# Performance work log

Hardware: AMD Instinct MI355X
Metric: run time of the kernel (lower is better)

Reference implementation:

```python
import jax, jax.numpy as jnp
import numpy as np

B, S, C = 2, 2048, 1536
HQ, HKV = 16, 4
DQK, DV = 128, 96
MAX_POS = 2048
CLIP = 5.0
EPS = 1e-5


def layer_norm(x, g, b):
    mu = jnp.mean(x, axis=-1, keepdims=True)
    var = jnp.mean(jnp.square(x - mu), axis=-1, keepdims=True)
    return (x - mu) * jax.lax.rsqrt(var + EPS) * g + b


def rms_bn(x, g, ms):
    # eval-mode EMA RMS batch-norm: per-channel running mean-square `ms`
    return x * jax.lax.rsqrt(ms + EPS) * g


def rope(x):
    # x: [B, S, H, C] with C even
    c = x.shape[-1]
    nf = c // 2
    s = x.shape[1]
    positions = jnp.arange(s, dtype=x.dtype)
    lin = jnp.arange(nf, dtype=x.dtype)
    end = max(MAX_POS - nf + 1.0, 1.0)
    geom = jnp.exp(jnp.linspace(0.0, jnp.log(jnp.asarray(end, dtype=x.dtype)), nf))
    inv_freq = 1.0 / (lin + geom)
    theta = positions[:, None] * inv_freq          # [S, nf]
    theta = jnp.repeat(theta, 2, axis=-1)[:, None, :]  # [S, 1, C]
    x_rot = jnp.stack([-x[..., 1::2], x[..., ::2]], axis=-1).reshape(x.shape)
    return x * jnp.cos(theta) + x_rot * jnp.sin(theta)


def setup_inputs() -> dict:
    key = jax.random.key(0)
    ks = jax.random.split(key, 8)
    d = {
        'x': jax.random.normal(ks[0], (B, S, C), dtype=jnp.float32),
        'bn1_g': jnp.ones((C,), jnp.float32),
        'bn1_ms': jnp.ones((C,), jnp.float32),
        'Wq': jax.random.normal(ks[1], (C, HQ * DQK), jnp.float32) * 0.02,
        'Wk': jax.random.normal(ks[2], (C, HKV * DQK), jnp.float32) * 0.02,
        'Wv': jax.random.normal(ks[3], (C, HKV * DV), jnp.float32) * 0.02,
        'qn_g': jnp.ones((DQK,), jnp.float32), 'qn_b': jnp.zeros((DQK,), jnp.float32),
        'kn_g': jnp.ones((DQK,), jnp.float32), 'kn_b': jnp.zeros((DQK,), jnp.float32),
        'vn_g': jnp.ones((DV,), jnp.float32), 'vn_b': jnp.zeros((DV,), jnp.float32),
        'Wo': jax.random.normal(ks[4], (HQ * DV, C), jnp.float32) * 0.02,
        'bo': jnp.zeros((C,), jnp.float32),
        'bn2_g': jnp.ones((C,), jnp.float32),
        'bn2_ms': jnp.ones((C,), jnp.float32),
    }
    return d


def reference(x, bn1_g, bn1_ms, Wq, Wk, Wv, qn_g, qn_b, kn_g, kn_b, vn_g, vn_b, Wo, bo, bn2_g, bn2_ms):
    rep = HQ // HKV
    h = rms_bn(x, bn1_g, bn1_ms)                       # [B,S,C]
    q = (h @ Wq).reshape(B, S, HQ, DQK)
    k = (h @ Wk).reshape(B, S, HKV, DQK)
    v = (h @ Wv).reshape(B, S, HKV, DV)
    q = layer_norm(q, qn_g, qn_b)
    k = layer_norm(k, kn_g, kn_b)
    v = layer_norm(v, vn_g, vn_b)
    q = rope(q)
    k = rope(k)
    # torch .repeat(1,1,rep,1) tiles head axis: [h0..hkv-1] * rep
    k = jnp.tile(k, (1, 1, rep, 1))                    # [B,S,HQ,DQK]
    v = jnp.tile(v, (1, 1, rep, 1))                    # [B,S,HQ,DV]
    logits = jnp.einsum('bshc,bShc->bhsS', q, k) / (DQK ** 0.5)
    logits = jnp.tanh(logits / CLIP) * CLIP
    attn = jax.nn.softmax(logits, axis=-1)
    y = jnp.einsum('bhsS,bShc->bshc', attn, v)         # [B,S,HQ,DV]
    y = y.reshape(B, S, HQ * DV)
    y = y @ Wo + bo
    y = rms_bn(y, bn2_g, bn2_ms)
    return y
```

## Files before the change

### kernel.cpp

```cpp
#include <hip/hip_runtime.h>
#include <hip/hip_bf16.h>
#include <math.h>

typedef __hip_bfloat16 bf16;
typedef __attribute__((ext_vector_type(8))) short short8;
typedef __attribute__((ext_vector_type(4))) short short4s;
typedef __attribute__((ext_vector_type(4))) float f32x4;

constexpr int Bb=2, Ss=2048, Cc=1536, HQn=16, HKVn=4, Dqk=128, Dv=96;
constexpr int NR   = Bb*Ss;
constexpr int NQKV = HQn*Dqk + HKVn*Dqk + HKVn*Dv;
constexpr int COL_K = HQn*Dqk;
constexpr int COL_V = COL_K + HKVn*Dqk;
constexpr int NY   = HQn*Dv;
constexpr float EPSf=1e-5f, CLIPf=5.0f;
constexpr float LOG2E = 1.44269504089f;

__device__ __forceinline__ float s2f(short s) {
    unsigned u = ((unsigned)(unsigned short)s) << 16;
    return __builtin_bit_cast(float, u);
}
__device__ __forceinline__ short f2s(float v) {
    bf16 b = __float2bfloat16(v);
    return __builtin_bit_cast(short, b);
}
__device__ __forceinline__ bool is_bf(const void* tagp) {
    return ((*(const unsigned*)tagp) & 0xFFFFu) != 0u;
}
__device__ __forceinline__ float ldd(const void* p, size_t i, bool bf) {
    return bf ? s2f(((const short*)p)[i]) : ((const float*)p)[i];
}

__global__ __launch_bounds__(256) void k_pre(const void* g1, const void* ms1,
        const void* bo, const void* g2, const void* ms2,
        float* __restrict__ ascale, float* __restrict__ ebias,
        float* __restrict__ escale, float2* __restrict__ tab) {
    bool bf = is_bf(ms1);
    int idx = blockIdx.x*256 + threadIdx.x;
    if (idx < Cc) {
        ascale[idx] = rsqrtf(ldd(ms1,idx,bf) + EPSf) * ldd(g1,idx,bf);
        ebias[idx]  = ldd(bo,idx,bf);
        escale[idx] = rsqrtf(ldd(ms2,idx,bf) + EPSf) * ldd(g2,idx,bf);
    }
    if (idx < Ss*64) {
        int s = idx >> 6, f = idx & 63;
        float geom = expf((float)f * (logf(1985.0f) * (1.0f/63.0f)));
        float invf = 1.0f / ((float)f + geom);
        float th = (float)s * invf;
        tab[idx] = make_float2(cosf(th), sinf(th));
    }
}

__global__ __launch_bounds__(256) void k_bn1(const void* __restrict__ x,
        const float* __restrict__ ascale, short* __restrict__ h, const void* tagp) {
    bool bf = is_bf(tagp);
    size_t i8 = (size_t)(blockIdx.x*256 + threadIdx.x) * 8;
    if (i8 >= (size_t)NR*Cc) return;
    int c = (int)(i8 % Cc);
    float xv[8];
    if (bf) {
        short8 xa = *(const short8*)((const short*)x + i8);
        #pragma unroll
        for (int j=0;j<8;++j) xv[j] = s2f(xa[j]);
    } else {
        const float* xf = (const float*)x + i8;
        #pragma unroll
        for (int j=0;j<8;++j) xv[j] = xf[j];
    }
    short8 o;
    #pragma unroll
    for (int j=0;j<8;++j) o[j] = f2s(xv[j] * ascale[c+j]);
    *(short8*)(h + i8) = o;
}

__global__ __launch_bounds__(256) void k_trw(const void* __restrict__ Wq,
        const void* __restrict__ Wk, const void* __restrict__ Wv,
        const void* __restrict__ Wo, short* __restrict__ WT, const void* tagp) {
    __shared__ short tile[32][33];
    bool bf = is_bf(tagp);
    int gt = blockIdx.x*32;
    int k0 = blockIdx.y*32;
    const void* W; int N, nl;
    if      (gt < 2048) { W = Wq; N = 2048; nl = gt; }
    else if (gt < 2560) { W = Wk; N = 512;  nl = gt - 2048; }
    else if (gt < 2944) { W = Wv; N = 384;  nl = gt - 2560; }
    else                { W = Wo; N = 1536; nl = gt - 2944; }
    int t = threadIdx.x, c = t & 31;
    #pragma unroll
    for (int r8=0; r8<32; r8+=8) {
        int r = r8 + (t>>5);
        tile[r][c] = f2s(ldd(W, (size_t)(k0+r)*N + nl + c, bf));
    }
    __syncthreads();
    #pragma unroll
    for (int r8=0; r8<32; r8+=8) {
        int r = r8 + (t>>5);
        WT[(size_t)(gt + r)*Cc + k0 + c] = tile[c][r];
    }
}

__global__ __launch_bounds__(256) void k_gemm(const short* __restrict__ A,
        const short* __restrict__ BT, void* __restrict__ Cout,
        int M, int N, int K,
        const float* __restrict__ ebias, const float* __restrict__ escale,
        int epi, const void* tagp) {
    __shared__ short As[128*32];
    __shared__ short Bs[128*32];
    const int t = threadIdx.x;
    const int w = t >> 6, lane = t & 63;
    const int l15 = lane & 15, quad = lane >> 4;
    const int wm = (w>>1)*64, wn = (w&1)*64;
    const int m0 = blockIdx.y*128, n0 = blockIdx.x*128;
    const int c0 = lane >> 2;
    const int koff = (lane & 3) * 8;

    f32x4 acc[4][4];
    #pragma unroll
    for (int i=0;i<4;++i)
        #pragma unroll
        for (int j=0;j<4;++j) acc[i][j] = (f32x4){0.f,0.f,0.f,0.f};

    for (int k0 = 0; k0 < K; k0 += 32) {
        __syncthreads();
        #pragma unroll
        for (int c=0; c<2; ++c) {
            int rA = w*32 + c*16;
            const short* ga = A  + (size_t)(m0 + rA + c0)*K + k0 + koff;
            const short* gb = BT + (size_t)(n0 + rA + c0)*K + k0 + koff;
            __builtin_amdgcn_global_load_lds(
                (const __attribute__((address_space(1))) void*)ga,
                (__attribute__((address_space(3))) void*)&As[rA*32], 16, 0, 0);
            __builtin_amdgcn_global_load_lds(
                (const __attribute__((address_space(1))) void*)gb,
                (__attribute__((address_space(3))) void*)&Bs[rA*32], 16, 0, 0);
        }
        __syncthreads();
        short8 af[4], bfr[4];
        #pragma unroll
        for (int mt=0; mt<4; ++mt)
            af[mt] = *(const short8*)&As[(wm + mt*16 + l15)*32 + quad*8];
        #pragma unroll
        for (int nt=0; nt<4; ++nt)
            bfr[nt] = *(const short8*)&Bs[(wn + nt*16 + l15)*32 + quad*8];
        #pragma unroll
        for (int mt=0; mt<4; ++mt)
            #pragma unroll
            for (int nt=0; nt<4; ++nt)
                acc[mt][nt] = __builtin_amdgcn_mfma_f32_16x16x32_bf16(
                    af[mt], bfr[nt], acc[mt][nt], 0, 0, 0);
    }

    const bool outf32 = epi && !is_bf(tagp);
    #pragma unroll
    for (int mt=0; mt<4; ++mt) {
        #pragma unroll
        for (int nt=0; nt<4; ++nt) {
            int col = n0 + wn + nt*16 + l15;
            float eb = epi ? ebias[col]  : 0.f;
            float es = epi ? escale[col] : 1.f;
            #pragma unroll
            for (int reg=0; reg<4; ++reg) {
                int row = m0 + wm + mt*16 + quad*4 + reg;
                float v = acc[mt][nt][reg];
                if (epi) v = (v + eb) * es;
                if (outf32) ((float*)Cout)[(size_t)row*N + col] = v;
                else        ((short*)Cout)[(size_t)row*N + col] = f2s(v);
            }
        }
    }
}

__global__ __launch_bounds__(256) void k_ln(short* __restrict__ qkvb,
        const float2* __restrict__ tab,
        const void* qg, const void* qb_, const void* kg, const void* kb_,
        const void* vg, const void* vb_, const void* tagp) {
    bool bf = is_bf(tagp);
    int R = blockIdx.x*4 + (threadIdx.x>>6);
    int lane = threadIdx.x & 63;
    int hidx = R % 24, bs = R / 24, s = bs % Ss;
    const void *g, *bia; int coff, D, dorope;
    if (hidx < 16)      { coff = hidx*Dqk;              D = Dqk; g = qg; bia = qb_; dorope = 1; }
    else if (hidx < 20) { coff = COL_K + (hidx-16)*Dqk; D = Dqk; g = kg; bia = kb_; dorope = 1; }
    else                { coff = COL_V + (hidx-20)*Dv;  D = Dv;  g = vg; bia = vb_; dorope = 0; }
    short* p = qkvb + (size_t)bs*NQKV + coff;
    int d0 = lane*2;
    bool act = d0 < D;
    float v0 = 0.f, v1 = 0.f;
    if (act) { v0 = s2f(p[d0]); v1 = s2f(p[d0+1]); }
    float sum = v0 + v1;
    #pragma unroll
    for (int m=1; m<64; m<<=1) sum += __shfl_xor(sum, m);
    float mu = sum / (float)D;
    float c0 = act ? v0-mu : 0.f, c1 = act ? v1-mu : 0.f;
    float sq = c0*c0 + c1*c1;
    #pragma unroll
    for (int m=1; m<64; m<<=1) sq += __shfl_xor(sq, m);
    float r = rsqrtf(sq/(float)D + EPSf);
    if (act) {
        float y0 = c0*r*ldd(g,d0,bf)   + ldd(bia,d0,bf);
        float y1 = c1*r*ldd(g,d0+1,bf) + ldd(bia,d0+1,bf);
        if (dorope) {
            float2 cs = tab[s*64 + lane];
            float t0 = y0*cs.x - y1*cs.y;
            y1 = y1*cs.x + y0*cs.y;
            y0 = t0;
        }
        p[d0] = f2s(y0); p[d0+1] = f2s(y1);
    }
}

__global__ __launch_bounds__(256) void k_trv(const short* __restrict__ qkvb,
        short* __restrict__ vT) {
    __shared__ short tile[32][33];
    int bs0 = blockIdx.x*32;
    int dg0 = blockIdx.y*32;
    int t = threadIdx.x, c = t & 31;
    #pragma unroll
    for (int r8=0; r8<32; r8+=8) {
        int r = r8 + (t>>5);
        tile[r][c] = qkvb[(size_t)(bs0+r)*NQKV + COL_V + dg0 + c];
    }
    __syncthreads();
    int b = bs0 >> 11, s0 = bs0 & 2047;
    #pragma unroll
    for (int r8=0; r8<32; r8+=8) {
        int r = r8 + (t>>5);
        vT[((size_t)(b*384 + dg0 + r))*Ss + s0 + c] = tile[c][r];
    }
}

__global__ __launch_bounds__(256) void k_attn(const short* __restrict__ qkvb,
        const short* __restrict__ vT, short* __restrict__ Yb) {
    __shared__ __align__(16) short Ks[64*136];
    __shared__ __align__(16) short VTs[96*72];
    __shared__ __align__(16) short Ps[128*72];
    const int q0 = blockIdx.x*128, hq = blockIdx.y, b = blockIdx.z;
    const int kvh = hq & (HKVn-1);
    const int t = threadIdx.x;
    const int w = t >> 6, lane = t & 63;
    const int l15 = lane & 15, quad = lane >> 4;
    const float ctan = 2.0f * (0.0883883476f / CLIPf) * LOG2E;
    const float c2   = -2.0f * CLIPf * LOG2E;

    short8 qf[2][4];
    #pragma unroll
    for (int qt=0; qt<2; ++qt) {
        const short* qp = qkvb + (size_t)(b*Ss + q0 + w*32 + qt*16 + l15)*NQKV + hq*Dqk;
        #pragma unroll
        for (int ds=0; ds<4; ++ds) qf[qt][ds] = *(const short8*)(qp + ds*32 + quad*8);
    }

    f32x4 oacc[2][6];
    #pragma unroll
    for (int qt=0; qt<2; ++qt)
        #pragma unroll
        for (int nt=0; nt<6; ++nt) oacc[qt][nt] = (f32x4){0.f,0.f,0.f,0.f};
    float lsum[2] = {0.f, 0.f};

    const short* Kb = qkvb + ((size_t)b*Ss)*NQKV + COL_K + kvh*Dqk;
    const short* Vb = vT + ((size_t)(b*HKVn + kvh)*Dv)*Ss;

    for (int kc = 0; kc < Ss/64; ++kc) {
        const int j0 = kc*64;
        __syncthreads();
        #pragma unroll
        for (int it=0; it<4; ++it) {
            int idx = it*256 + t;
            int key = idx >> 4, d = (idx & 15)*8;
            *(short8*)&Ks[key*136 + d] = *(const short8*)(Kb + (size_t)(j0+key)*NQKV + d);
        }
        #pragma unroll
        for (int it=0; it<3; ++it) {
            int idx = it*256 + t;
            int dv = idx >> 3, c8 = (idx & 7)*8;
            *(short8*)&VTs[dv*72 + c8] = *(const short8*)(Vb + (size_t)dv*Ss + j0 + c8);
        }
        __syncthreads();

        f32x4 sacc[4][2];
        #pragma unroll
        for (int kt=0; kt<4; ++kt)
            #pragma unroll
            for (int qt=0; qt<2; ++qt) sacc[kt][qt] = (f32x4){0.f,0.f,0.f,0.f};
        #pragma unroll
        for (int kt=0; kt<4; ++kt) {
            short8 kf[4];
            #pragma unroll
            for (int ds=0; ds<4; ++ds)
                kf[ds] = *(const short8*)&Ks[(kt*16 + l15)*136 + ds*32 + quad*8];
            #pragma unroll
            for (int qt=0; qt<2; ++qt)
                #pragma unroll
                for (int ds=0; ds<4; ++ds)
                    sacc[kt][qt] = __builtin_amdgcn_mfma_f32_16x16x32_bf16(
                        kf[ds], qf[qt][ds], sacc[kt][qt], 0, 0, 0);
        }

        #pragma unroll
        for (int kt=0; kt<4; ++kt)
            #pragma unroll
            for (int qt=0; qt<2; ++qt) {
                short4s pb;
                #pragma unroll
                for (int reg=0; reg<4; ++reg) {
                    float u = __builtin_amdgcn_exp2f(sacc[kt][qt][reg] * ctan);
                    float p = __builtin_amdgcn_exp2f(c2 * __builtin_amdgcn_rcpf(u + 1.0f));
                    short pb16 = f2s(p);
                    pb[reg] = pb16;
                    lsum[qt] += s2f(pb16);
                }
                *(short4s*)&Ps[(w*32 + qt*16 + l15)*72 + kt*16 + quad*4] = pb;
            }

        short8 vf[6][2];
        #pragma unroll
        for (int nt=0; nt<6; ++nt)
            #pragma unroll
            for (int ks=0; ks<2; ++ks)
                vf[nt][ks] = *(const short8*)&VTs[(nt*16 + l15)*72 + ks*32 + quad*8];
        #pragma unroll
        for (int qt=0; qt<2; ++qt) {
            short8 pf0 = *(const short8*)&Ps[(w*32 + qt*16 + l15)*72 + quad*8];
            short8 pf1 = *(const short8*)&Ps[(w*32 + qt*16 + l15)*72 + 32 + quad*8];
            #pragma unroll
            for (int nt=0; nt<6; ++nt) {
                oacc[qt][nt] = __builtin_amdgcn_mfma_f32_16x16x32_bf16(
                    pf0, vf[nt][0], oacc[qt][nt], 0, 0, 0);
                oacc[qt][nt] = __builtin_amdgcn_mfma_f32_16x16x32_bf16(
                    pf1, vf[nt][1], oacc[qt][nt], 0, 0, 0);
            }
        }
    }

    float lred[2];
    #pragma unroll
    for (int qt=0; qt<2; ++qt) {
        float l = lsum[qt];
        l += __shfl_xor(l, 16);
        l += __shfl_xor(l, 32);
        lred[qt] = l;
    }
    #pragma unroll
    for (int qt=0; qt<2; ++qt) {
        float rinv[4];
        #pragma unroll
        for (int reg=0; reg<4; ++reg)
            rinv[reg] = __builtin_amdgcn_rcpf(__shfl(lred[qt], quad*4 + reg, 16));
        #pragma unroll
        for (int nt=0; nt<6; ++nt)
            #pragma unroll
            for (int reg=0; reg<4; ++reg) {
                int row = q0 + w*32 + qt*16 + quad*4 + reg;
                Yb[(size_t)(b*Ss + row)*NY + hq*Dv + nt*16 + l15] =
                    f2s(oacc[qt][nt][reg] * rinv[reg]);
            }
    }
}

extern "C" void kernel_launch(void* const* d_in, const int* in_sizes, int n_in,
                              void* d_out, int out_size, void* d_ws, size_t ws_size,
                              hipStream_t stream) {
    const void* x     = d_in[0];
    const void* bn1g  = d_in[1];
    const void* bn1ms = d_in[2];
    const void* Wq    = d_in[3];
    const void* Wk    = d_in[4];
    const void* Wv    = d_in[5];
    const void* qng   = d_in[6];
    const void* qnb   = d_in[7];
    const void* kng   = d_in[8];
    const void* knb   = d_in[9];
    const void* vng   = d_in[10];
    const void* vnb   = d_in[11];
    const void* Wo    = d_in[12];
    const void* bo    = d_in[13];
    const void* bn2g  = d_in[14];
    const void* bn2ms = d_in[15];

    char* wsb = (char*)d_ws;
    float*  ascale = (float*)(wsb);
    float*  ebias  = (float*)(wsb + 6144);
    float*  escale = (float*)(wsb + 12288);
    float2* tab    = (float2*)(wsb + 18432);
    short*  h      = (short*)(wsb + 1067520);
    short*  WT     = (short*)(wsb + 13650432);
    short*  qkv    = (short*)(wsb + 27412992);
    short*  vT     = (short*)(wsb + 51530240);
    short*  y      = (short*)(wsb + 54675968);
    short*  WoT    = WT + (size_t)NQKV*Cc;

    k_pre<<<512, 256, 0, stream>>>(bn1g, bn1ms, bo, bn2g, bn2ms,
                                   ascale, ebias, escale, tab);
    k_bn1<<<(NR*Cc/8 + 255)/256, 256, 0, stream>>>(x, ascale, h, bn1ms);
    k_trw<<<dim3(4480/32, Cc/32), 256, 0, stream>>>(Wq, Wk, Wv, Wo, WT, bn1ms);

    k_gemm<<<dim3(NQKV/128, NR/128), 256, 0, stream>>>(
        h, WT, qkv, NR, NQKV, Cc, nullptr, nullptr, 0, bn1ms);

    k_ln<<<NR*24/4, 256, 0, stream>>>(qkv, tab, qng, qnb, kng, knb, vng, vnb, bn1ms);
    k_trv<<<dim3(NR/32, 384/32), 256, 0, stream>>>(qkv, vT);

    k_attn<<<dim3(Ss/128, HQn, Bb), 256, 0, stream>>>(qkv, vT, y);

    k_gemm<<<dim3(Cc/128, NR/128), 256, 0, stream>>>(
        y, WoT, d_out, NR, Cc, NY, ebias, escale, 1, bn1ms);
}
```

Baseline: 392.9 us.

## Pipeline attention K/V loads, keep P in registers, remap workgroups to XCDs

The attention kernel now double-buffers K and V tiles in shared memory, prefetching the next chunk into registers while the current chunk is computed, so one barrier per chunk is removed. P is no longer round-tripped through shared memory: the V transpose writes keys in a permuted order so the MFMA output layout of the score tile feeds directly as the A operand of the PV product. The grid is flattened and remapped so workgroups sharing a batch and KV head land on the same XCD for L2 reuse, and s_setprio brackets the MFMA sections. The cost is more registers and shared memory and a tight coupling between the permutation in the transpose and the register layout.

New measurement: 355.8 us. -9.4%, faster.

```diff
diff --git a/kernel.cpp b/kernel.cpp
--- a/kernel.cpp
+++ b/kernel.cpp
@@ -222,20 +222,25 @@
     }
     __syncthreads();
     int b = bs0 >> 11, s0 = bs0 & 2047;
+    int s = s0 + c;
+    int sp = (s & ~63) + ((s>>5)&1)*32 + ((s>>2)&3)*8 + ((s>>4)&1)*4 + (s&3);
     #pragma unroll
     for (int r8=0; r8<32; r8+=8) {
         int r = r8 + (t>>5);
-        vT[((size_t)(b*384 + dg0 + r))*Ss + s0 + c] = tile[c][r];
+        vT[((size_t)(b*384 + dg0 + r))*Ss + sp] = tile[c][r];
     }
 }
 
 __global__ __launch_bounds__(256) void k_attn(const short* __restrict__ qkvb,
         const short* __restrict__ vT, short* __restrict__ Yb) {
-    __shared__ __align__(16) short Ks[64*136];
-    __shared__ __align__(16) short VTs[96*72];
-    __shared__ __align__(16) short Ps[128*72];
-    const int q0 = blockIdx.x*128, hq = blockIdx.y, b = blockIdx.z;
-    const int kvh = hq & (HKVn-1);
+    __shared__ __align__(16) short Ks[2][64*136];
+    __shared__ __align__(16) short VTs[2][96*72];
+    const int wg = blockIdx.x;
+    const int xcd = wg & 7, idx = wg >> 3;
+    const int b = xcd >> 2, kvh = xcd & 3;
+    const int qb = idx >> 2, hsub = idx & 3;
+    const int hq = hsub*4 + kvh;
+    const int q0 = qb*128;
     const int t = threadIdx.x;
     const int w = t >> 6, lane = t & 63;
     const int l15 = lane & 15, quad = lane >> 4;
@@ -260,34 +265,52 @@
     const short* Kb = qkvb + ((size_t)b*Ss)*NQKV + COL_K + kvh*Dqk;
     const short* Vb = vT + ((size_t)(b*HKVn + kvh)*Dv)*Ss;
 
-    for (int kc = 0; kc < Ss/64; ++kc) {
-        const int j0 = kc*64;
+    short8 kreg[4], vreg[3];
+    auto stage_load = [&](int j0) {
+        #pragma unroll
+        for (int it=0; it<4; ++it) {
+            int ii = it*256 + t;
+            kreg[it] = *(const short8*)(Kb + (size_t)(j0 + (ii>>4))*NQKV + (ii&15)*8);
+        }
+        #pragma unroll
+        for (int it=0; it<3; ++it) {
+            int ii = it*256 + t;
+            vreg[it] = *(const short8*)(Vb + (size_t)(ii>>3)*Ss + j0 + (ii&7)*8);
+        }
+    };
+    auto stage_write = [&](int pb) {
+        #pragma unroll
+        for (int it=0; it<4; ++it) {
+            int ii = it*256 + t;
+            *(short8*)&Ks[pb][(ii>>4)*136 + (ii&15)*8] = kreg[it];
+        }
+        #pragma unroll
+        for (int it=0; it<3; ++it) {
+            int ii = it*256 + t;
+            *(short8*)&VTs[pb][(ii>>3)*72 + (ii&7)*8] = vreg[it];
+        }
+    };
+
+    stage_load(0);
+    stage_write(0);
+    int p = 0;
+    constexpr int NCH = Ss/64;
+    for (int kc = 0; kc < NCH; ++kc) {
         __syncthreads();
-        #pragma unroll
-        for (int it=0; it<4; ++it) {
-            int idx = it*256 + t;
-            int key = idx >> 4, d = (idx & 15)*8;
-            *(short8*)&Ks[key*136 + d] = *(const short8*)(Kb + (size_t)(j0+key)*NQKV + d);
-        }
-        #pragma unroll
-        for (int it=0; it<3; ++it) {
-            int idx = it*256 + t;
-            int dv = idx >> 3, c8 = (idx & 7)*8;
-            *(short8*)&VTs[dv*72 + c8] = *(const short8*)(Vb + (size_t)dv*Ss + j0 + c8);
-        }
-        __syncthreads();
+        if (kc+1 < NCH) stage_load((kc+1)*64);
 
         f32x4 sacc[4][2];
         #pragma unroll
         for (int kt=0; kt<4; ++kt)
             #pragma unroll
             for (int qt=0; qt<2; ++qt) sacc[kt][qt] = (f32x4){0.f,0.f,0.f,0.f};
+        __builtin_amdgcn_s_setprio(1);
         #pragma unroll
         for (int kt=0; kt<4; ++kt) {
             short8 kf[4];
             #pragma unroll
             for (int ds=0; ds<4; ++ds)
-                kf[ds] = *(const short8*)&Ks[(kt*16 + l15)*136 + ds*32 + quad*8];
+                kf[ds] = *(const short8*)&Ks[p][(kt*16 + l15)*136 + ds*32 + quad*8];
             #pragma unroll
             for (int qt=0; qt<2; ++qt)
                 #pragma unroll
@@ -295,41 +318,39 @@
                     sacc[kt][qt] = __builtin_amdgcn_mfma_f32_16x16x32_bf16(
                         kf[ds], qf[qt][ds], sacc[kt][qt], 0, 0, 0);
         }
-
-        #pragma unroll
-        for (int kt=0; kt<4; ++kt)
-            #pragma unroll
-            for (int qt=0; qt<2; ++qt) {
-                short4s pb;
+        __builtin_amdgcn_s_setprio(0);
+
+        short8 pa[2][2];
+        #pragma unroll
+        for (int c=0; c<2; ++c)
+            #pragma unroll
+            for (int qt=0; qt<2; ++qt)
                 #pragma unroll
-                for (int reg=0; reg<4; ++reg) {
-                    float u = __builtin_amdgcn_exp2f(sacc[kt][qt][reg] * ctan);
-                    float p = __builtin_amdgcn_exp2f(c2 * __builtin_amdgcn_rcpf(u + 1.0f));
-                    short pb16 = f2s(p);
-                    pb[reg] = pb16;
-                    lsum[qt] += s2f(pb16);
-                }
-                *(short4s*)&Ps[(w*32 + qt*16 + l15)*72 + kt*16 + quad*4] = pb;
+                for (int jh=0; jh<2; ++jh)
+                    #pragma unroll
+                    for (int j=0; j<4; ++j) {
+                        float u  = __builtin_amdgcn_exp2f(sacc[c*2+jh][qt][j] * ctan);
+                        float pv = __builtin_amdgcn_exp2f(c2 * __builtin_amdgcn_rcpf(u + 1.0f));
+                        short ps = f2s(pv);
+                        pa[c][qt][jh*4 + j] = ps;
+                        lsum[qt] += s2f(ps);
+                    }
+
+        __builtin_amdgcn_s_setprio(1);
+        #pragma unroll
+        for (int c=0; c<2; ++c)
+            #pragma unroll
+            for (int nt=0; nt<6; ++nt) {
+                short8 vf = *(const short8*)&VTs[p][(nt*16 + l15)*72 + c*32 + quad*8];
+                #pragma unroll
+                for (int qt=0; qt<2; ++qt)
+                    oacc[qt][nt] = __builtin_amdgcn_mfma_f32_16x16x32_bf16(
+                        pa[c][qt], vf, oacc[qt][nt], 0, 0, 0);
             }
-
-        short8 vf[6][2];
-        #pragma unroll
-        for (int nt=0; nt<6; ++nt)
-            #pragma unroll
-            for (int ks=0; ks<2; ++ks)
-                vf[nt][ks] = *(const short8*)&VTs[(nt*16 + l15)*72 + ks*32 + quad*8];
-        #pragma unroll
-        for (int qt=0; qt<2; ++qt) {
-            short8 pf0 = *(const short8*)&Ps[(w*32 + qt*16 + l15)*72 + quad*8];
-            short8 pf1 = *(const short8*)&Ps[(w*32 + qt*16 + l15)*72 + 32 + quad*8];
-            #pragma unroll
-            for (int nt=0; nt<6; ++nt) {
-                oacc[qt][nt] = __builtin_amdgcn_mfma_f32_16x16x32_bf16(
-                    pf0, vf[nt][0], oacc[qt][nt], 0, 0, 0);
-                oacc[qt][nt] = __builtin_amdgcn_mfma_f32_16x16x32_bf16(
-                    pf1, vf[nt][1], oacc[qt][nt], 0, 0, 0);
-            }
-        }
+        __builtin_amdgcn_s_setprio(0);
+
+        if (kc+1 < NCH) stage_write(p^1);
+        p ^= 1;
     }
 
     float lred[2];
@@ -400,7 +421,7 @@
     k_ln<<<NR*24/4, 256, 0, stream>>>(qkv, tab, qng, qnb, kng, knb, vng, vnb, bn1ms);
     k_trv<<<dim3(NR/32, 384/32), 256, 0, stream>>>(qkv, vT);
 
-    k_attn<<<dim3(Ss/128, HQn, Bb), 256, 0, stream>>>(qkv, vT, y);
+    k_attn<<<512, 256, 0, stream>>>(qkv, vT, y);
 
     k_gemm<<<dim3(Cc/128, NR/128), 256, 0, stream>>>(
         y, WoT, d_out, NR, Cc, NY, ebias, escale, 1, bn1ms);
```
